# Performance work log

Measured on AMD Instinct MI355X. Metric: run time of the kernel, lower is better.

Reference implementation:

```python
import jax, jax.numpy as jnp
import numpy as np

H = 128
IN = 5
EPS = 1e-5


def lstm(x, Wih, Whh, bih, bhh):
    # x: [B,T,D]; PyTorch gate order i,f,g,o along 4H axis
    B, T, _ = x.shape
    xW = jnp.einsum('btd,gd->btg', x, Wih) + bih + bhh  # [B,T,4H]
    WhhT = Whh.T

    def step(carry, xt):
        h, c = carry
        g = xt + h @ WhhT
        i, f, gg, o = jnp.split(g, 4, axis=-1)
        i = jax.nn.sigmoid(i)
        f = jax.nn.sigmoid(f)
        gg = jnp.tanh(gg)
        o = jax.nn.sigmoid(o)
        c = f * c + i * gg
        h = o * jnp.tanh(c)
        return (h, c), h

    h0 = jnp.zeros((B, H), x.dtype)
    _, hs = jax.lax.scan(step, (h0, h0), jnp.swapaxes(xW, 0, 1))
    return jnp.swapaxes(hs, 0, 1)  # [B,T,H]


def batchnorm(x, gamma, beta):
    # training-mode BN over (batch, time) per channel; x: [B,T,H]
    mean = jnp.mean(x, axis=(0, 1))
    var = jnp.var(x, axis=(0, 1))
    return (x - mean) * (gamma * jax.lax.rsqrt(var + EPS)) + beta


def forward_one(x, Wih1, Whh1, bih1, bhh1, g1, b1, Wih2, Whh2, bih2, bhh2, g2, b2, fcW, fcb):
    out = lstm(x, Wih1, Whh1, bih1, bhh1)
    out = batchnorm(out, g1, b1)
    # dropout is identity (eval / deterministic reference)
    out = lstm(out, Wih2, Whh2, bih2, bhh2)
    out = batchnorm(out, g2, b2)
    emb = out[:, -1, :] @ fcW.T + fcb  # [B,128]
    norm = jnp.sqrt(jnp.sum(emb * emb, axis=1, keepdims=True))
    return emb / jnp.maximum(norm, 1e-12)  # F.normalize p=2


def setup_inputs() -> dict:
    key = jax.random.key(0)
    ks = jax.random.split(key, 20)
    B, T = 512, 128
    s_in = 1.0 / np.sqrt(H)
    d = {
        'a': jax.random.normal(ks[0], (B, T, IN), jnp.float32),
        'p': jax.random.normal(ks[1], (B, T, IN), jnp.float32),
        'n': jax.random.normal(ks[2], (B, T, IN), jnp.float32),
        'Wih1': jax.random.uniform(ks[3], (4 * H, IN), jnp.float32, -s_in, s_in),
        'Whh1': jax.random.uniform(ks[4], (4 * H, H), jnp.float32, -s_in, s_in),
        'bih1': jax.random.uniform(ks[5], (4 * H,), jnp.float32, -s_in, s_in),
        'bhh1': jax.random.uniform(ks[6], (4 * H,), jnp.float32, -s_in, s_in),
        'g1': jnp.ones((H,), jnp.float32),
        'b1': jnp.zeros((H,), jnp.float32),
        'Wih2': jax.random.uniform(ks[7], (4 * H, H), jnp.float32, -s_in, s_in),
        'Whh2': jax.random.uniform(ks[8], (4 * H, H), jnp.float32, -s_in, s_in),
        'bih2': jax.random.uniform(ks[9], (4 * H,), jnp.float32, -s_in, s_in),
        'bhh2': jax.random.uniform(ks[10], (4 * H,), jnp.float32, -s_in, s_in),
        'g2': jnp.ones((H,), jnp.float32),
        'b2': jnp.zeros((H,), jnp.float32),
        'fcW': jax.random.uniform(ks[11], (H, H), jnp.float32, -s_in, s_in),
        'fcb': jax.random.uniform(ks[12], (H,), jnp.float32, -s_in, s_in),
    }
    return d


def reference(a, p, n, Wih1, Whh1, bih1, bhh1, g1, b1, Wih2, Whh2, bih2, bhh2, g2, b2, fcW, fcb):
    f = lambda x: forward_one(x, Wih1, Whh1, bih1, bhh1, g1, b1, Wih2, Whh2, bih2, bhh2, g2, b2, fcW, fcb)
    return (f(a), f(p), f(n))
```

## Files before the change

kernel.cpp:

```cpp
#include <hip/hip_runtime.h>


typedef __attribute__((ext_vector_type(8))) _Float16 half8;
typedef __attribute__((ext_vector_type(4))) float f32x4;

#define TS 128
#define HID 128
#define NGATE 512
#define INV_N (1.0f/65536.0f)

#define BAR() asm volatile("s_waitcnt lgkmcnt(0)\n\ts_barrier" ::: "memory")

__device__ __forceinline__ float rcpf(float x) { return __builtin_amdgcn_rcpf(x); }
__device__ __forceinline__ float clamp20(float x) { return fminf(fmaxf(x, -20.0f), 20.0f); }

__device__ __forceinline__ _Float16 lstm_cell(float zi, float zf, float zg, float zo,
                                              float& c) {
  zg = clamp20(zg);
  float ei = __expf(-zi);
  float eg = __expf(-2.0f * zg);
  float ef = __expf(-zf);
  float fv = rcpf(1.0f + ef);
  float ig = (1.0f - eg) * rcpf((1.0f + ei) * (1.0f + eg));
  float cc = fv * c + ig;
  c = cc;
  float ccl = clamp20(cc);
  float eo = __expf(-zo);
  float ec = __expf(-2.0f * ccl);
  float hv = (1.0f - ec) * rcpf((1.0f + eo) * (1.0f + ec));
  return (_Float16)hv;
}


__global__ __launch_bounds__(512, 2) void lstm1_kernel(
    const float* __restrict__ xa, const float* __restrict__ xp,
    const float* __restrict__ xn,
    const float* __restrict__ Wih1, const float* __restrict__ Whh1,
    const float* __restrict__ bih1, const float* __restrict__ bhh1,
    _Float16* __restrict__ hs1,
    float* __restrict__ s1sum, float* __restrict__ s1sq) {
  const int wg = blockIdx.x;
  const int inp = wg >> 5;
  const int tid = threadIdx.x;
  const int w = tid >> 6;
  const int lane = tid & 63;
  const int l15 = lane & 15;
  const int quad = lane >> 4;
  const int col = w * 16 + l15;
  const int kb = quad * 8;

  __shared__ _Float16 hb[2][2048];
  __shared__ _Float16 xt[TS][128];

  const float* x = (inp == 0) ? xa : ((inp == 1) ? xp : xn);
  const int rloc = (wg & 31) * 16;

  for (int i = tid; i < 4096; i += 512) ((_Float16*)hb)[i] = (_Float16)0.0f;
  for (int i = tid; i < TS * 128; i += 512) ((_Float16*)xt)[i] = (_Float16)0.0f;
  __syncthreads();
  for (int i = tid; i < 10240; i += 512) {
    int r = i / 640, rem = i - r * 640;
    int t = rem / 5, d = rem - t * 5;
    xt[t][r * 8 + d] = (_Float16)x[(rloc + r) * 640 + rem];
  }

  half8 bh[4][4];
#pragma unroll
  for (int kt = 0; kt < 4; ++kt)
#pragma unroll
    for (int gt = 0; gt < 4; ++gt) {
      const float* src = &Whh1[(gt * 128 + col) * HID + kt * 32 + kb];
      half8 v;
#pragma unroll
      for (int j = 0; j < 8; ++j) v[j] = (_Float16)src[j];
      bh[kt][gt] = v;
    }
  half8 bx[4];
#pragma unroll
  for (int gt = 0; gt < 4; ++gt) {
    half8 v = {0, 0, 0, 0, 0, 0, 0, 0};
    if (quad == 0) {
#pragma unroll
      for (int j = 0; j < 5; ++j) v[j] = (_Float16)Wih1[(gt * 128 + col) * 5 + j];
    }
    bx[gt] = v;
  }
  f32x4 biasv[4];
#pragma unroll
  for (int gt = 0; gt < 4; ++gt) {
    float b = bih1[gt * 128 + col] + bhh1[gt * 128 + col];
    biasv[gt][0] = b; biasv[gt][1] = b; biasv[gt][2] = b; biasv[gt][3] = b;
  }

  const int rbase = (quad * 16 + l15) * 8;
  const int wbase = (w >> 1) * 512 + ((w & 1) * 2 + (l15 >> 3)) * 128 +
                    quad * 32 + (l15 & 7);
  _Float16* hs1w = hs1 + (size_t)wg * TS * 2048;

  float c[4] = {0, 0, 0, 0};
  float ssum = 0.0f, ssq = 0.0f;
  __syncthreads();

  half8 xv = {0, 0, 0, 0, 0, 0, 0, 0};
  if (quad == 0) xv = *(const half8*)&xt[0][l15 * 8];

  for (int t = 0; t < TS; ++t) {
    f32x4 acc[4];
#pragma unroll
    for (int gt = 0; gt < 4; ++gt)
      acc[gt] = __builtin_amdgcn_mfma_f32_16x16x32_f16(xv, bx[gt], biasv[gt], 0, 0, 0);
    if (t + 1 < TS && quad == 0)
      xv = *(const half8*)&xt[t + 1][l15 * 8];
    BAR();
    if (t > 0) {
      float2 cp = *(const float2*)&hb[t & 1][tid * 4];
      *(float2*)&hs1w[(size_t)(t - 1) * 2048 + tid * 4] = cp;
    }
#pragma unroll
    for (int kt = 0; kt < 4; ++kt) {
      half8 ah = *(const half8*)&hb[t & 1][kt * 512 + rbase];
#pragma unroll
      for (int gt = 0; gt < 4; ++gt)
        acc[gt] = __builtin_amdgcn_mfma_f32_16x16x32_f16(ah, bh[kt][gt], acc[gt], 0, 0, 0);
    }
    const int wb = (t + 1) & 1;
#pragma unroll
    for (int r = 0; r < 4; ++r) {
      _Float16 hh = lstm_cell(acc[0][r], acc[1][r], acc[2][r], acc[3][r], c[r]);
      float hr = (float)hh;
      ssum += hr; ssq += hr * hr;
      hb[wb][wbase + r * 8] = hh;
    }
  }
  BAR();
  {
    float2 cp = *(const float2*)&hb[0][tid * 4];
    *(float2*)&hs1w[(size_t)(TS - 1) * 2048 + tid * 4] = cp;
  }
  float s = ssum, q = ssq;
  s += __shfl_xor(s, 16); s += __shfl_xor(s, 32);
  q += __shfl_xor(q, 16); q += __shfl_xor(q, 32);
  if (quad == 0) {
    atomicAdd(&s1sum[inp * HID + col], s);
    atomicAdd(&s1sq[inp * HID + col], q);
  }
}

__global__ __launch_bounds__(512, 2) void lstm2_kernel(
    const _Float16* __restrict__ hs1,
    const float* __restrict__ Wih2, const float* __restrict__ Whh2,
    const float* __restrict__ bih2, const float* __restrict__ bhh2,
    const float* __restrict__ g1, const float* __restrict__ b1,
    const float* __restrict__ s1sum, const float* __restrict__ s1sq,
    _Float16* __restrict__ hlast,
    float* __restrict__ s2sum, float* __restrict__ s2sq) {
  const int wg = blockIdx.x;
  const int inp = wg >> 5;
  const int tid = threadIdx.x;
  const int w = tid >> 6;
  const int lane = tid & 63;
  const int l15 = lane & 15;
  const int quad = lane >> 4;
  const int col = w * 16 + l15;
  const int kb = quad * 8;

  __shared__ _Float16 hb[2][2048];
  __shared__ float scale1L[128], shift1L[128];

  if (tid < 128) {
    float sm = s1sum[inp * HID + tid];
    float sq = s1sq[inp * HID + tid];
    float m = sm * INV_N;
    float v = sq * INV_N - m * m;
    float sc = g1[tid] * rsqrtf(v + 1e-5f);
    scale1L[tid] = sc;
    shift1L[tid] = b1[tid] - m * sc;
  }
  for (int i = tid; i < 4096; i += 512) ((_Float16*)hb)[i] = (_Float16)0.0f;
  __syncthreads();

  half8 bh[4][4], bxw[4][4];
#pragma unroll
  for (int kt = 0; kt < 4; ++kt)
#pragma unroll
    for (int gt = 0; gt < 4; ++gt) {
      const float* ph = &Whh2[(gt * 128 + col) * HID + kt * 32 + kb];
      const float* px = &Wih2[(gt * 128 + col) * HID + kt * 32 + kb];
      half8 vh, vx;
#pragma unroll
      for (int j = 0; j < 8; ++j) {
        vh[j] = (_Float16)ph[j];
        vx[j] = (_Float16)(scale1L[kt * 32 + kb + j] * px[j]);
      }
      bh[kt][gt] = vh;
      bxw[kt][gt] = vx;
    }
  f32x4 biasv[4];
#pragma unroll
  for (int gt = 0; gt < 4; ++gt) {
    int gcol = gt * 128 + col;
    float b = bih2[gcol] + bhh2[gcol];
    const float* pw = &Wih2[gcol * HID];
    for (int h = 0; h < HID; ++h) b += shift1L[h] * pw[h];
    biasv[gt][0] = b; biasv[gt][1] = b; biasv[gt][2] = b; biasv[gt][3] = b;
  }

  const int rbase = (quad * 16 + l15) * 8;
  const int wbase = (w >> 1) * 512 + ((w & 1) * 2 + (l15 >> 3)) * 128 +
                    quad * 32 + (l15 & 7);
  const _Float16* hg = hs1 + (size_t)wg * TS * 2048;

  half8 a2A[4], a2B[4];
#pragma unroll
  for (int kt = 0; kt < 4; ++kt) {
    a2A[kt] = *(const half8*)&hg[kt * 512 + rbase];
    a2B[kt] = *(const half8*)&hg[(size_t)2048 + kt * 512 + rbase];
  }

  float c[4] = {0, 0, 0, 0};
  float ssum = 0.0f, ssq = 0.0f;

  auto step = [&](int t, half8 (&cur)[4]) {
    f32x4 acc[4];
#pragma unroll
    for (int gt = 0; gt < 4; ++gt)
      acc[gt] = __builtin_amdgcn_mfma_f32_16x16x32_f16(cur[0], bxw[0][gt], biasv[gt], 0, 0, 0);
#pragma unroll
    for (int kt = 1; kt < 4; ++kt)
#pragma unroll
      for (int gt = 0; gt < 4; ++gt)
        acc[gt] = __builtin_amdgcn_mfma_f32_16x16x32_f16(cur[kt], bxw[kt][gt], acc[gt], 0, 0, 0);
    if (t + 2 < TS) {
#pragma unroll
      for (int kt = 0; kt < 4; ++kt)
        cur[kt] = *(const half8*)&hg[(size_t)(t + 2) * 2048 + kt * 512 + rbase];
    }
    BAR();
#pragma unroll
    for (int kt = 0; kt < 4; ++kt) {
      half8 ah = *(const half8*)&hb[t & 1][kt * 512 + rbase];
#pragma unroll
      for (int gt = 0; gt < 4; ++gt)
        acc[gt] = __builtin_amdgcn_mfma_f32_16x16x32_f16(ah, bh[kt][gt], acc[gt], 0, 0, 0);
    }
    const int wb = (t + 1) & 1;
#pragma unroll
    for (int r = 0; r < 4; ++r) {
      _Float16 hh = lstm_cell(acc[0][r], acc[1][r], acc[2][r], acc[3][r], c[r]);
      float hr = (float)hh;
      ssum += hr; ssq += hr * hr;
      hb[wb][wbase + r * 8] = hh;
    }
  };

  for (int t = 0; t < TS; t += 2) {
    step(t, a2A);
    step(t + 1, a2B);
  }

  BAR();
  {
    float2 cp = *(const float2*)&hb[0][tid * 4];
    *(float2*)&hlast[(size_t)wg * 2048 + tid * 4] = cp;
  }
  float s = ssum, q = ssq;
  s += __shfl_xor(s, 16); s += __shfl_xor(s, 32);
  q += __shfl_xor(q, 16); q += __shfl_xor(q, 32);
  if (quad == 0) {
    atomicAdd(&s2sum[inp * HID + col], s);
    atomicAdd(&s2sq[inp * HID + col], q);
  }
}

__global__ __launch_bounds__(256, 1) void head_kernel(
    const _Float16* __restrict__ hlast,
    const float* __restrict__ s2sum, const float* __restrict__ s2sq,
    const float* __restrict__ g2, const float* __restrict__ b2,
    const float* __restrict__ fcW, const float* __restrict__ fcb,
    float* __restrict__ out) {
  const int wg = blockIdx.x;
  const int inp = wg >> 5;
  const int gr0 = wg * 16;
  const int tid = threadIdx.x;

  __shared__ float fcwT[128][132];
  __shared__ float bnh[16][132];
  __shared__ float s2[128], sh2[128];
  __shared__ float part[16][16];
  __shared__ float inv[16];

  if (tid < 128) {
    float m = s2sum[inp * HID + tid] * INV_N;
    float v = s2sq[inp * HID + tid] * INV_N - m * m;
    float s = g2[tid] * rsqrtf(v + 1e-5f);
    s2[tid] = s; sh2[tid] = b2[tid] - m * s;
  }
  for (int i = tid; i < 16384; i += 256) {
    int j = i >> 7, h = i & 127;
    fcwT[h][j] = fcW[i];
  }
  __syncthreads();
  {
    int row = tid >> 4, c0 = (tid & 15) * 8;
#pragma unroll
    for (int k = 0; k < 8; ++k) {
      int h = c0 + k;
      int ad = ((h >> 5) << 9) + (((h >> 3) & 3) << 7) + (row << 3) + (h & 7);
      bnh[row][h] = (float)hlast[(size_t)wg * 2048 + ad] * s2[h] + sh2[h];
    }
  }
  __syncthreads();
  const int row = tid >> 4, jl = tid & 15;
  float emb[8];
  float sq = 0.0f;
#pragma unroll
  for (int jj = 0; jj < 8; ++jj) {
    int j = jl + jj * 16;
    float acc = fcb[j];
    for (int h = 0; h < HID; ++h) acc += bnh[row][h] * fcwT[h][j];
    emb[jj] = acc; sq += acc * acc;
  }
  part[row][jl] = sq;
  __syncthreads();
  if (tid < 16) {
    float s = 0.0f;
    for (int k = 0; k < 16; ++k) s += part[tid][k];
    inv[tid] = 1.0f / fmaxf(sqrtf(s), 1e-12f);
  }
  __syncthreads();
#pragma unroll
  for (int jj = 0; jj < 8; ++jj)
    out[(size_t)(gr0 + row) * HID + jl + jj * 16] = emb[jj] * inv[row];
}

extern "C" void kernel_launch(void* const* d_in, const int* in_sizes, int n_in,
                              void* d_out, int out_size, void* d_ws, size_t ws_size,
                              hipStream_t stream) {
  const float* a    = (const float*)d_in[0];
  const float* p    = (const float*)d_in[1];
  const float* nn   = (const float*)d_in[2];
  const float* Wih1 = (const float*)d_in[3];
  const float* Whh1 = (const float*)d_in[4];
  const float* bih1 = (const float*)d_in[5];
  const float* bhh1 = (const float*)d_in[6];
  const float* g1   = (const float*)d_in[7];
  const float* b1   = (const float*)d_in[8];
  const float* Wih2 = (const float*)d_in[9];
  const float* Whh2 = (const float*)d_in[10];
  const float* bih2 = (const float*)d_in[11];
  const float* bhh2 = (const float*)d_in[12];
  const float* g2   = (const float*)d_in[13];
  const float* b2   = (const float*)d_in[14];
  const float* fcW  = (const float*)d_in[15];
  const float* fcb  = (const float*)d_in[16];

  char* ws = (char*)d_ws;
  float* s1sum = (float*)(ws + 0);
  float* s1sq  = (float*)(ws + 1536);
  float* s2sum = (float*)(ws + 3072);
  float* s2sq  = (float*)(ws + 4608);
  _Float16* hlast = (_Float16*)(ws + 8192);
  _Float16* hs1   = (_Float16*)(ws + 401408);

  hipMemsetAsync(ws, 0, 6144, stream);

  lstm1_kernel<<<96, 512, 0, stream>>>(a, p, nn, Wih1, Whh1, bih1, bhh1,
                                       hs1, s1sum, s1sq);
  lstm2_kernel<<<96, 512, 0, stream>>>(hs1, Wih2, Whh2, bih2, bhh2, g1, b1,
                                       s1sum, s1sq, hlast, s2sum, s2sq);
  head_kernel<<<96, 256, 0, stream>>>(hlast, s2sum, s2sq, g2, b2, fcW, fcb,
                                      (float*)d_out);
}
```

Baseline: 407.5 us.

## Replace BN stat atomics with partial sums and precompute folded LSTM2 weights in mid kernel

Per-workgroup BN partial sums are written to distinct slots instead of atomically added, which removes the memset launch and the atomic contention. A new mid kernel reduces the layer-1 stats, folds the BN scale into fp16 Wih2 and the BN shift into an effective bias once per input, so lstm2 no longer recomputes these in each of its 96 workgroups. This adds one kernel launch and a strided (non-coalesced) fp16 weight gather in lstm2's prologue. The head kernel now reduces 32 partials per channel.

```diff
diff --git a/kernel.cpp b/kernel.cpp
--- a/kernel.cpp
+++ b/kernel.cpp
@@ -38,7 +38,7 @@
     const float* __restrict__ Wih1, const float* __restrict__ Whh1,
     const float* __restrict__ bih1, const float* __restrict__ bhh1,
     _Float16* __restrict__ hs1,
-    float* __restrict__ s1sum, float* __restrict__ s1sq) {
+    float* __restrict__ s1part, float* __restrict__ s1qpart) {
   const int wg = blockIdx.x;
   const int inp = wg >> 5;
   const int tid = threadIdx.x;
@@ -141,19 +141,67 @@
   s += __shfl_xor(s, 16); s += __shfl_xor(s, 32);
   q += __shfl_xor(q, 16); q += __shfl_xor(q, 32);
   if (quad == 0) {
-    atomicAdd(&s1sum[inp * HID + col], s);
-    atomicAdd(&s1sq[inp * HID + col], q);
+    s1part[wg * HID + col] = s;
+    s1qpart[wg * HID + col] = q;
+  }
+}
+
+__global__ void mid_kernel(const float* __restrict__ s1part, const float* __restrict__ s1qpart,
+                           const float* __restrict__ g1, const float* __restrict__ b1,
+                           const float* __restrict__ Wih2,
+                           const float* __restrict__ bih2, const float* __restrict__ bhh2,
+                           _Float16* __restrict__ w2s, float* __restrict__ bias2eff) {
+  int bid = blockIdx.x, tid = threadIdx.x;
+  if (bid < 768) {
+    int i0 = bid * 256;
+    int inp = i0 >> 16, k = (i0 & 65535) >> 9;
+    __shared__ float red[65];
+    if (tid < 32) {
+      red[tid] = s1part[(inp * 32 + tid) * HID + k];
+      red[32 + tid] = s1qpart[(inp * 32 + tid) * HID + k];
+    }
+    __syncthreads();
+    if (tid == 0) {
+      float sm = 0.0f, sq = 0.0f;
+      for (int j = 0; j < 32; ++j) { sm += red[j]; sq += red[32 + j]; }
+      float m = sm * INV_N;
+      float v = sq * INV_N - m * m;
+      red[64] = g1[k] * rsqrtf(v + 1e-5f);
+    }
+    __syncthreads();
+    float sc = red[64];
+    int i = i0 + tid, g = i & 511;
+    w2s[i] = (_Float16)(sc * Wih2[g * HID + k]);
+  } else {
+    int i = (bid - 768) * 256 + tid;
+    int inp = i >> 9, g = i & 511;
+    __shared__ float sc[128], sh[128];
+    if (tid < 128) {
+      float sm = 0.0f, sq = 0.0f;
+      for (int j = 0; j < 32; ++j) {
+        sm += s1part[(inp * 32 + j) * HID + tid];
+        sq += s1qpart[(inp * 32 + j) * HID + tid];
+      }
+      float m = sm * INV_N;
+      float v = sq * INV_N - m * m;
+      float s = g1[tid] * rsqrtf(v + 1e-5f);
+      sc[tid] = s;
+      sh[tid] = b1[tid] - m * s;
+    }
+    __syncthreads();
+    float acc = bih2[g] + bhh2[g];
+    for (int h = 0; h < HID; ++h) acc += sh[h] * Wih2[g * HID + h];
+    bias2eff[i] = acc;
   }
 }
 
 __global__ __launch_bounds__(512, 2) void lstm2_kernel(
     const _Float16* __restrict__ hs1,
-    const float* __restrict__ Wih2, const float* __restrict__ Whh2,
-    const float* __restrict__ bih2, const float* __restrict__ bhh2,
-    const float* __restrict__ g1, const float* __restrict__ b1,
-    const float* __restrict__ s1sum, const float* __restrict__ s1sq,
+    const _Float16* __restrict__ w2s,
+    const float* __restrict__ Whh2,
+    const float* __restrict__ bias2eff,
     _Float16* __restrict__ hlast,
-    float* __restrict__ s2sum, float* __restrict__ s2sq) {
+    float* __restrict__ s2part, float* __restrict__ s2qpart) {
   const int wg = blockIdx.x;
   const int inp = wg >> 5;
   const int tid = threadIdx.x;
@@ -165,32 +213,21 @@
   const int kb = quad * 8;
 
   __shared__ _Float16 hb[2][2048];
-  __shared__ float scale1L[128], shift1L[128];
-
-  if (tid < 128) {
-    float sm = s1sum[inp * HID + tid];
-    float sq = s1sq[inp * HID + tid];
-    float m = sm * INV_N;
-    float v = sq * INV_N - m * m;
-    float sc = g1[tid] * rsqrtf(v + 1e-5f);
-    scale1L[tid] = sc;
-    shift1L[tid] = b1[tid] - m * sc;
-  }
   for (int i = tid; i < 4096; i += 512) ((_Float16*)hb)[i] = (_Float16)0.0f;
-  __syncthreads();
-
+
+  const _Float16* w2sI = w2s + (size_t)inp * HID * NGATE;
   half8 bh[4][4], bxw[4][4];
 #pragma unroll
   for (int kt = 0; kt < 4; ++kt)
 #pragma unroll
     for (int gt = 0; gt < 4; ++gt) {
-      const float* ph = &Whh2[(gt * 128 + col) * HID + kt * 32 + kb];
-      const float* px = &Wih2[(gt * 128 + col) * HID + kt * 32 + kb];
+      int gcol = gt * 128 + col;
+      const float* ph = &Whh2[(size_t)gcol * HID + kt * 32 + kb];
       half8 vh, vx;
 #pragma unroll
       for (int j = 0; j < 8; ++j) {
         vh[j] = (_Float16)ph[j];
-        vx[j] = (_Float16)(scale1L[kt * 32 + kb + j] * px[j]);
+        vx[j] = w2sI[(kt * 32 + kb + j) * NGATE + gcol];
       }
       bh[kt][gt] = vh;
       bxw[kt][gt] = vx;
@@ -198,10 +235,7 @@
   f32x4 biasv[4];
 #pragma unroll
   for (int gt = 0; gt < 4; ++gt) {
-    int gcol = gt * 128 + col;
-    float b = bih2[gcol] + bhh2[gcol];
-    const float* pw = &Wih2[gcol * HID];
-    for (int h = 0; h < HID; ++h) b += shift1L[h] * pw[h];
+    float b = bias2eff[inp * NGATE + gt * 128 + col];
     biasv[gt][0] = b; biasv[gt][1] = b; biasv[gt][2] = b; biasv[gt][3] = b;
   }
 
@@ -219,6 +253,8 @@
 
   float c[4] = {0, 0, 0, 0};
   float ssum = 0.0f, ssq = 0.0f;
+
+  __syncthreads();
 
   auto step = [&](int t, half8 (&cur)[4]) {
     f32x4 acc[4];
@@ -267,14 +303,14 @@
   s += __shfl_xor(s, 16); s += __shfl_xor(s, 32);
   q += __shfl_xor(q, 16); q += __shfl_xor(q, 32);
   if (quad == 0) {
-    atomicAdd(&s2sum[inp * HID + col], s);
-    atomicAdd(&s2sq[inp * HID + col], q);
+    s2part[wg * HID + col] = s;
+    s2qpart[wg * HID + col] = q;
   }
 }
 
 __global__ __launch_bounds__(256, 1) void head_kernel(
     const _Float16* __restrict__ hlast,
-    const float* __restrict__ s2sum, const float* __restrict__ s2sq,
+    const float* __restrict__ s2part, const float* __restrict__ s2qpart,
     const float* __restrict__ g2, const float* __restrict__ b2,
     const float* __restrict__ fcW, const float* __restrict__ fcb,
     float* __restrict__ out) {
@@ -290,8 +326,13 @@
   __shared__ float inv[16];
 
   if (tid < 128) {
-    float m = s2sum[inp * HID + tid] * INV_N;
-    float v = s2sq[inp * HID + tid] * INV_N - m * m;
+    float sm = 0.0f, sq = 0.0f;
+    for (int j = 0; j < 32; ++j) {
+      sm += s2part[(inp * 32 + j) * HID + tid];
+      sq += s2qpart[(inp * 32 + j) * HID + tid];
+    }
+    float m = sm * INV_N;
+    float v = sq * INV_N - m * m;
     float s = g2[tid] * rsqrtf(v + 1e-5f);
     s2[tid] = s; sh2[tid] = b2[tid] - m * s;
   }
@@ -355,19 +396,22 @@
   const float* fcb  = (const float*)d_in[16];
 
   char* ws = (char*)d_ws;
-  float* s1sum = (float*)(ws + 0);
-  float* s1sq  = (float*)(ws + 1536);
-  float* s2sum = (float*)(ws + 3072);
-  float* s2sq  = (float*)(ws + 4608);
-  _Float16* hlast = (_Float16*)(ws + 8192);
-  _Float16* hs1   = (_Float16*)(ws + 401408);
-
-  hipMemsetAsync(ws, 0, 6144, stream);
+  float* s1part  = (float*)(ws + 0);
+  float* s1qpart = (float*)(ws + 49152);
+  float* s2part  = (float*)(ws + 98304);
+  float* s2qpart = (float*)(ws + 147456);
+  _Float16* w2s   = (_Float16*)(ws + 196608);
+  float* bias2eff = (float*)(ws + 589824);
+  _Float16* hlast = (_Float16*)(ws + 595968);
+  _Float16* hs1   = (_Float16*)(ws + 989184);
+
 
   lstm1_kernel<<<96, 512, 0, stream>>>(a, p, nn, Wih1, Whh1, bih1, bhh1,
-                                       hs1, s1sum, s1sq);
-  lstm2_kernel<<<96, 512, 0, stream>>>(hs1, Wih2, Whh2, bih2, bhh2, g1, b1,
-                                       s1sum, s1sq, hlast, s2sum, s2sq);
-  head_kernel<<<96, 256, 0, stream>>>(hlast, s2sum, s2sq, g2, b2, fcW, fcb,
+                                       hs1, s1part, s1qpart);
+  mid_kernel<<<774, 256, 0, stream>>>(s1part, s1qpart, g1, b1, Wih2, bih2, bhh2,
+                                      w2s, bias2eff);
+  lstm2_kernel<<<96, 512, 0, stream>>>(hs1, w2s, Whh2, bias2eff,
+                                       hlast, s2part, s2qpart);
+  head_kernel<<<96, 256, 0, stream>>>(hlast, s2part, s2qpart, g2, b2, fcW, fcb,
                                       (float*)d_out);
 }
```

New measurement: 375.1 us. -7.9%, faster.
